# Kernel optimization log

Hardware: AMD Instinct MI355X
Metric: run time of the kernel (lower is better)

The kernel has to match this reference:

```python
import jax, jax.numpy as jnp
import numpy as np

H = 16
D_MODEL = 1024
D_K = D_MODEL // H
L = 4096


def setup_inputs() -> dict:
    key = jax.random.key(0)
    ks = jax.random.split(key, 11)
    s = 1.0 / np.sqrt(D_MODEL)
    inp = {
        "query": jax.random.normal(ks[0], (L, D_MODEL), dtype=jnp.float32),
        "key": jax.random.normal(ks[1], (L, D_MODEL), dtype=jnp.float32),
        "value": jax.random.normal(ks[2], (L, D_MODEL), dtype=jnp.float32),
        "Wq": jax.random.uniform(ks[3], (D_MODEL, D_MODEL), jnp.float32, -s, s),
        "Wk": jax.random.uniform(ks[4], (D_MODEL, D_MODEL), jnp.float32, -s, s),
        "Wv": jax.random.uniform(ks[5], (D_MODEL, D_MODEL), jnp.float32, -s, s),
        "Wo": jax.random.uniform(ks[6], (D_MODEL, D_MODEL), jnp.float32, -s, s),
        "bq": jax.random.uniform(ks[7], (D_MODEL,), jnp.float32, -s, s),
        "bk": jax.random.uniform(ks[8], (D_MODEL,), jnp.float32, -s, s),
        "bv": jax.random.uniform(ks[9], (D_MODEL,), jnp.float32, -s, s),
        "bo": jax.random.uniform(ks[10], (D_MODEL,), jnp.float32, -s, s),
    }
    return inp


def reference(query, key, value, Wq, Wk, Wv, Wo, bq, bk, bv, bo):
    # projections: torch Linear computes x @ W.T + b
    def proj(x, W, b):
        # [L, d_model] -> [h, L, d_k]
        y = x @ W.T + b
        return y.reshape(L, H, D_K).transpose(1, 0, 2)

    q = proj(query, Wq, bq)   # [h, L, d_k]
    k = proj(key, Wk, bk)
    v = proj(value, Wv, bv)

    scores = jnp.einsum("hqd,hkd->hqk", q, k) / jnp.sqrt(jnp.float32(D_K))  # [h, L, L]
    p = jax.nn.softmax(scores, axis=-1)
    x = jnp.einsum("hqk,hkd->hqd", p, v)         # [h, L, d_k]
    x = x.transpose(1, 0, 2).reshape(L, H * D_K)  # [L, d_model]
    return x @ Wo.T + bo
```

## Files before the change

kernel.cpp:

```cpp
#include <hip/hip_runtime.h>

#define L_SEQ 4096
#define DM 1024
#define NH 16
#define DK 64

typedef short s16x8 __attribute__((ext_vector_type(8)));
typedef float f32x4 __attribute__((ext_vector_type(4)));
typedef float f32x8 __attribute__((ext_vector_type(8)));
typedef float f32x16 __attribute__((ext_vector_type(16)));
typedef unsigned short u16t;
typedef unsigned int u32t;

typedef __attribute__((address_space(1))) unsigned int as1_u32;
typedef __attribute__((address_space(3))) unsigned int as3_u32;

#define GLOAD_LDS16(gsrc, ldst) \
  __builtin_amdgcn_global_load_lds((as1_u32*)(gsrc), (as3_u32*)(ldst), 16, 0, 0)

__device__ __forceinline__ u16t f2bf(float f) {
  union { float f; unsigned u; } v; v.f = f;
  unsigned u = v.u;
  u += 0x7fffu + ((u >> 16) & 1u);
  return (u16t)(u >> 16);
}

__device__ __forceinline__ float fexp2(float x) {
  float r;
  asm("v_exp_f32 %0, %1" : "=v"(r) : "v"(x));
  return r;
}

__device__ __forceinline__ float bflo(u32t u) {
  union { u32t u; float f; } v; v.u = u << 16; return v.f;
}
__device__ __forceinline__ float bfhi(u32t u) {
  union { u32t u; float f; } v; v.u = u & 0xffff0000u; return v.f;
}

struct CvtArgs { const float* s[7]; u16t* d[7]; };

__global__ __launch_bounds__(256) void cvt_all(CvtArgs a) {
  int g = blockIdx.x * 256 + threadIdx.x;
  int seg, off;
  if (g < 1572864) { seg = g >> 19;               off = g & 524287; }
  else             { int t = g - 1572864; seg = 3 + (t >> 17); off = t & 131071; }
  const float* src = a.s[seg] + (size_t)off * 8;
  u16t* dst = a.d[seg] + (size_t)off * 8;
  float4 x = *(const float4*)(src);
  float4 y = *(const float4*)(src + 4);
  uint4 o;
  o.x = (u32t)f2bf(x.x) | ((u32t)f2bf(x.y) << 16);
  o.y = (u32t)f2bf(x.z) | ((u32t)f2bf(x.w) << 16);
  o.z = (u32t)f2bf(y.x) | ((u32t)f2bf(y.y) << 16);
  o.w = (u32t)f2bf(y.z) | ((u32t)f2bf(y.w) << 16);
  *(uint4*)dst = o;
}

struct QkvArgs {
  const u16t* A[3]; const u16t* Bm[3]; const float* bias[3]; u16t* C[3];
  float scale0;
};

__global__ __launch_bounds__(256)
void gemm_qkv(QkvArgs ga) {
  __shared__ unsigned char lds[3][16384];
  const int flat = blockIdx.x;
  const int bid = (flat & 7) * 96 + (flat >> 3);
  const int z = bid >> 8;
  const int b = bid & 255;
  const int bc = (z == 2) ? (b & 31) : (b & 7);
  const int br = (z == 2) ? (b >> 5) : (b >> 3);
  const int N  = (z == 2) ? L_SEQ : DM;
  const float osc = (z == 0) ? ga.scale0 : 1.0f;
  const bool rowb = (z == 2);
  const u16t* A = ga.A[z];
  const u16t* Bm = ga.Bm[z];
  const float* bias = ga.bias[z];
  u16t* C = ga.C[z];
  const int K = DM;

  const int tid = threadIdx.x;
  const int lane = tid & 63;
  const int wv = tid >> 6;
  const int wr = wv >> 1, wc = wv & 1;
  const int l15 = lane & 15, l4 = lane >> 4;

  const int r_st = tid >> 2;
  const int c_st = (tid & 3) ^ ((r_st >> 1) & 3);
  const u16t* a0 = A + (size_t)(br * 128 + r_st) * K + c_st * 8;
  const u16t* a1 = a0 + (size_t)64 * K;
  const u16t* b0 = Bm + (size_t)(bc * 128 + r_st) * K + c_st * 8;
  const u16t* b1 = b0 + (size_t)64 * K;
  const int woff = wv * 1024;

  f32x4 acc[4][4] = {};

  auto stage = [&](int buf, int k0) {
    GLOAD_LDS16(a0 + k0, &lds[buf][woff]);
    GLOAD_LDS16(a1 + k0, &lds[buf][4096 + woff]);
    GLOAD_LDS16(b0 + k0, &lds[buf][8192 + woff]);
    GLOAD_LDS16(b1 + k0, &lds[buf][12288 + woff]);
  };

  auto compute = [&](int buf) {
    s16x8 af[4], bfr[4];
    #pragma unroll
    for (int m = 0; m < 4; ++m) {
      int r = wr * 64 + m * 16 + l15;
      int sl = l4 ^ ((r >> 1) & 3);
      af[m] = *(const s16x8*)&lds[buf][r * 64 + (sl << 4)];
    }
    #pragma unroll
    for (int n = 0; n < 4; ++n) {
      int r = wc * 64 + n * 16 + l15;
      int sl = l4 ^ ((r >> 1) & 3);
      bfr[n] = *(const s16x8*)&lds[buf][8192 + r * 64 + (sl << 4)];
    }
    #pragma unroll
    for (int m = 0; m < 4; ++m)
      #pragma unroll
      for (int n = 0; n < 4; ++n)
        acc[m][n] = __builtin_amdgcn_mfma_f32_16x16x32_bf16(af[m], bfr[n], acc[m][n], 0, 0, 0);
  };

  stage(0, 0);
  stage(1, 32);
  int t = 0;
  #pragma unroll 1
  for (int c = 0; c < 10; ++c) {
    #pragma unroll
    for (int ph = 0; ph < 3; ++ph) {
      asm volatile("s_waitcnt vmcnt(4)" ::: "memory");
      __builtin_amdgcn_s_barrier();
      __builtin_amdgcn_sched_barrier(0);
      stage((t + 2) % 3, (t + 2) * 32);
      compute(t % 3);
      ++t;
    }
  }
  asm volatile("s_waitcnt vmcnt(4)" ::: "memory");
  __builtin_amdgcn_s_barrier();
  __builtin_amdgcn_sched_barrier(0);
  compute(0);
  asm volatile("s_waitcnt vmcnt(0)" ::: "memory");
  __builtin_amdgcn_s_barrier();
  __builtin_amdgcn_sched_barrier(0);
  compute(1);

  const int l15p = rowb ? ((l15 & 3) | ((l15 & 4) << 1) | ((l15 & 8) >> 1)) : l15;

  #pragma unroll
  for (int m = 0; m < 4; ++m) {
    #pragma unroll
    for (int n = 0; n < 4; ++n) {
      #pragma unroll
      for (int i = 0; i < 4; ++i) {
        int row = br * 128 + wr * 64 + m * 16 + l4 * 4 + i;
        int col = bc * 128 + wc * 64 + n * 16 + l15p;
        float v = (acc[m][n][i] + (rowb ? bias[row] : bias[col])) * osc;
        C[(size_t)row * N + col] = f2bf(v);
      }
    }
  }
}

__global__ __launch_bounds__(256)
void gemm_out(const u16t* __restrict__ A, const u16t* __restrict__ B,
              const float* __restrict__ bias, float* __restrict__ C,
              int M, int N, int K) {
  __shared__ unsigned char lds[3][12288];
  const int tid = threadIdx.x;
  const int lane = tid & 63;
  const int wv = tid >> 6;
  const int wr = wv >> 1, wc = wv & 1;
  const int l15 = lane & 15, l4 = lane >> 4;
  const int flat = blockIdx.x + (blockIdx.y << 4);
  const int nsw = (flat & 7) * 64 + (flat >> 3);
  const int bc = nsw & 15, br = nsw >> 4;

  const int r_st = tid >> 2;
  const int c_st = (tid & 3) ^ ((r_st >> 1) & 3);
  const u16t* a0 = A + (size_t)(br * 128 + r_st) * K + c_st * 8;
  const u16t* a1 = a0 + (size_t)64 * K;
  const u16t* b0 = B + (size_t)(bc * 64 + r_st) * K + c_st * 8;
  const int woff = wv * 1024;

  f32x4 acc[4][2] = {};

  auto stage = [&](int buf, int k0) {
    GLOAD_LDS16(a0 + k0, &lds[buf][woff]);
    GLOAD_LDS16(a1 + k0, &lds[buf][4096 + woff]);
    GLOAD_LDS16(b0 + k0, &lds[buf][8192 + woff]);
  };

  auto compute = [&](int buf) {
    s16x8 af[4], bfr[2];
    #pragma unroll
    for (int m = 0; m < 4; ++m) {
      int r = wr * 64 + m * 16 + l15;
      int sl = l4 ^ ((r >> 1) & 3);
      af[m] = *(const s16x8*)&lds[buf][r * 64 + (sl << 4)];
    }
    #pragma unroll
    for (int n = 0; n < 2; ++n) {
      int r = wc * 32 + n * 16 + l15;
      int sl = l4 ^ ((r >> 1) & 3);
      bfr[n] = *(const s16x8*)&lds[buf][8192 + r * 64 + (sl << 4)];
    }
    #pragma unroll
    for (int m = 0; m < 4; ++m)
      #pragma unroll
      for (int n = 0; n < 2; ++n)
        acc[m][n] = __builtin_amdgcn_mfma_f32_16x16x32_bf16(af[m], bfr[n], acc[m][n], 0, 0, 0);
  };

  stage(0, 0);
  stage(1, 32);
  int t = 0;
  #pragma unroll 1
  for (int c = 0; c < 10; ++c) {
    #pragma unroll
    for (int ph = 0; ph < 3; ++ph) {
      asm volatile("s_waitcnt vmcnt(3)" ::: "memory");
      __builtin_amdgcn_s_barrier();
      __builtin_amdgcn_sched_barrier(0);
      stage((t + 2) % 3, (t + 2) * 32);
      compute(t % 3);
      ++t;
    }
  }
  asm volatile("s_waitcnt vmcnt(3)" ::: "memory");
  __builtin_amdgcn_s_barrier();
  __builtin_amdgcn_sched_barrier(0);
  compute(0);
  asm volatile("s_waitcnt vmcnt(0)" ::: "memory");
  __builtin_amdgcn_s_barrier();
  __builtin_amdgcn_sched_barrier(0);
  compute(1);

  #pragma unroll
  for (int m = 0; m < 4; ++m) {
    #pragma unroll
    for (int n = 0; n < 2; ++n) {
      #pragma unroll
      for (int i = 0; i < 4; ++i) {
        int row = br * 128 + wr * 64 + m * 16 + l4 * 4 + i;
        int col = bc * 64 + wc * 32 + n * 16 + l15;
        C[(size_t)row * N + col] = acc[m][n][i] + bias[col];
      }
    }
  }
}

#define PKBF(dst, a, b) \
  asm("v_cvt_pk_bf16_f32 %0, %1, %2" : "=v"(dst) : "v"(a), "v"(b))

#define MAKE_FRAG(S, B, FR) { \
    union { u32t u[4]; s16x8 v; } uu; \
    PKBF(uu.u[0], S[B + 0], S[B + 1]); \
    PKBF(uu.u[1], S[B + 2], S[B + 3]); \
    PKBF(uu.u[2], S[B + 4], S[B + 5]); \
    PKBF(uu.u[3], S[B + 6], S[B + 7]); \
    FR = uu.v; }

__global__ __launch_bounds__(512, 4)
void attn_fused(const u16t* __restrict__ Qp, const u16t* __restrict__ Kp,
                const u16t* __restrict__ VpT, u16t* __restrict__ Op,
                float* __restrict__ Ml) {
  __shared__ unsigned char sStage[3][16384];

  const int tid = threadIdx.x;
  const int lane = tid & 63;
  const int w = tid >> 6;
  const int l31 = lane & 31;
  const int hi = lane >> 5;
  const int flat = blockIdx.x;
  const int nsw = (flat & 7) * 64 + (flat >> 3);
  const int qt = nsw & 15;
  const int h = (nsw >> 4) & 15;
  const int z = nsw >> 8;
  const int kvbase = z * (L_SEQ / 2);
  const int qrow = qt * 256 + w * 32 + l31;
  u16t* Opz = Op + (size_t)z * (L_SEQ * DM);
  float* Mlz = Ml + z * (NH * L_SEQ);

  s16x8 qf[4];
  {
    const u16t* qsrc = Qp + (size_t)qrow * DM + h * DK + hi * 8;
    #pragma unroll
    for (int c = 0; c < 4; ++c) qf[c] = *(const s16x8*)(qsrc + c * 16);
  }

  f32x16 acc0 = {}, acc1 = {};
  float lrow = 0.f;

  const u16t* kptr = Kp + (size_t)(kvbase + lane) * DM + h * DK + w * 8;
  const u16t* vptr = VpT + (size_t)(h * DK + lane) * L_SEQ + kvbase + w * 8;
  const int woffK = w * 1024;

  auto stage = [&](int buf) {
    GLOAD_LDS16(kptr, &sStage[buf][woffK]);
    GLOAD_LDS16(vptr, &sStage[buf][8192 + woffK]);
    kptr += 64 * DM;
    vptr += 64;
  };

  const int rdoff = (hi << 10) + (l31 << 4);

  auto compute = [&](const unsigned char* sb) {
    f32x16 st0 = {}, st1 = {};
    __builtin_amdgcn_s_setprio(1);
    #pragma unroll
    for (int c = 0; c < 4; ++c) {
      s16x8 kf0 = *(const s16x8*)(sb + c * 2048);
      s16x8 kf1 = *(const s16x8*)(sb + c * 2048 + 512);
      st0 = __builtin_amdgcn_mfma_f32_32x32x16_bf16(kf0, qf[c], st0, 0, 0, 0);
      st1 = __builtin_amdgcn_mfma_f32_32x32x16_bf16(kf1, qf[c], st1, 0, 0, 0);
    }
    __builtin_amdgcn_s_setprio(0);

    #pragma unroll
    for (int r = 0; r < 16; ++r) {
      st0[r] = fexp2(st0[r]);
      st1[r] = fexp2(st1[r]);
    }
    f32x16 sv = st0 + st1;
    f32x8 s8v = __builtin_shufflevector(sv, sv, 0, 1, 2, 3, 4, 5, 6, 7) +
                __builtin_shufflevector(sv, sv, 8, 9, 10, 11, 12, 13, 14, 15);
    f32x4 s4v = __builtin_shufflevector(s8v, s8v, 0, 1, 2, 3) +
                __builtin_shufflevector(s8v, s8v, 4, 5, 6, 7);
    lrow += (s4v[0] + s4v[1]) + (s4v[2] + s4v[3]);

    __builtin_amdgcn_s_setprio(1);
    #pragma unroll
    for (int cc = 0; cc < 4; ++cc) {
      s16x8 pfr;
      if (cc == 0)      MAKE_FRAG(st0, 0, pfr)
      else if (cc == 1) MAKE_FRAG(st0, 8, pfr)
      else if (cc == 2) MAKE_FRAG(st1, 0, pfr)
      else              MAKE_FRAG(st1, 8, pfr)
      s16x8 vf0 = *(const s16x8*)(sb + 8192 + cc * 2048);
      s16x8 vf1 = *(const s16x8*)(sb + 8192 + cc * 2048 + 512);
      acc0 = __builtin_amdgcn_mfma_f32_32x32x16_bf16(vf0, pfr, acc0, 0, 0, 0);
      acc1 = __builtin_amdgcn_mfma_f32_32x32x16_bf16(vf1, pfr, acc1, 0, 0, 0);
    }
    __builtin_amdgcn_s_setprio(0);
  };

  auto phase = [&](int bc, int bs) {
    asm volatile("s_waitcnt vmcnt(2)" ::: "memory");
    __builtin_amdgcn_s_barrier();
    __builtin_amdgcn_sched_barrier(0);
    stage(bs);
    compute(sStage[bc] + rdoff);
  };

  stage(0);
  stage(1);
  #pragma unroll 1
  for (int c = 0; c < 10; ++c) {
    phase(0, 2);
    phase(1, 0);
    phase(2, 1);
  }
  asm volatile("s_waitcnt vmcnt(2)" ::: "memory");
  __builtin_amdgcn_s_barrier();
  __builtin_amdgcn_sched_barrier(0);
  compute(sStage[0] + rdoff);
  asm volatile("s_waitcnt vmcnt(0)" ::: "memory");
  __builtin_amdgcn_s_barrier();
  __builtin_amdgcn_sched_barrier(0);
  compute(sStage[1] + rdoff);

  lrow += __shfl_xor(lrow, 32);
  u16t* orow = Opz + (size_t)qrow * DM + h * DK;
  #pragma unroll
  for (int rq = 0; rq < 4; ++rq) {
    union { u16t h4[4]; uint2 v; } p0, p1;
    #pragma unroll
    for (int i = 0; i < 4; ++i) {
      p0.h4[i] = f2bf(acc0[4 * rq + i]);
      p1.h4[i] = f2bf(acc1[4 * rq + i]);
    }
    int d0 = 8 * rq + 4 * hi;
    *(uint2*)(orow + d0)      = p0.v;
    *(uint2*)(orow + 32 + d0) = p1.v;
  }
  if (hi == 0) Mlz[h * L_SEQ + qrow] = lrow;
}

__global__ __launch_bounds__(256)
void attn_combine(const u16t* __restrict__ Op, const float* __restrict__ Ml,
                  u16t* __restrict__ AO) {
  int g = blockIdx.x * 256 + threadIdx.x;
  int qh = g >> 2;
  int d0 = (g & 3) * 16;
  int q = qh >> 4, h = qh & 15;
  size_t off = (size_t)q * DM + h * DK + d0;
  const size_t OSTR = (size_t)L_SEQ * DM;

  int mi = h * L_SEQ + q;
  float inv = 1.0f / (Ml[mi] + Ml[NH * L_SEQ + mi]);

  uint4 a[2], b[2], o[2];
  a[0] = *(const uint4*)(Op + off);         a[1] = *(const uint4*)(Op + off + 8);
  b[0] = *(const uint4*)(Op + OSTR + off);  b[1] = *(const uint4*)(Op + OSTR + off + 8);
  #pragma unroll
  for (int k = 0; k < 2; ++k) {
    u32t* au = (u32t*)&a[k]; u32t* bu = (u32t*)&b[k]; u32t* ou = (u32t*)&o[k];
    #pragma unroll
    for (int j = 0; j < 4; ++j) {
      float lo = (bflo(au[j]) + bflo(bu[j])) * inv;
      float hf = (bfhi(au[j]) + bfhi(bu[j])) * inv;
      ou[j] = (u32t)f2bf(lo) | ((u32t)f2bf(hf) << 16);
    }
  }
  *(uint4*)(AO + off)     = o[0];
  *(uint4*)(AO + off + 8) = o[1];
}

extern "C" void kernel_launch(void* const* d_in, const int* in_sizes, int n_in,
                              void* d_out, int out_size, void* d_ws, size_t ws_size,
                              hipStream_t stream) {
  const float* query = (const float*)d_in[0];
  const float* key_  = (const float*)d_in[1];
  const float* value = (const float*)d_in[2];
  const float* Wq = (const float*)d_in[3];
  const float* Wk = (const float*)d_in[4];
  const float* Wv = (const float*)d_in[5];
  const float* Wo = (const float*)d_in[6];
  const float* bq = (const float*)d_in[7];
  const float* bk = (const float*)d_in[8];
  const float* bv = (const float*)d_in[9];
  const float* bo = (const float*)d_in[10];

  char* ws = (char*)d_ws;
  const size_t MB = 1u << 20;
  u16t* qb  = (u16t*)(ws + 0 * MB);
  u16t* kb  = (u16t*)(ws + 8 * MB);
  u16t* vb  = (u16t*)(ws + 16 * MB);
  u16t* wqb = (u16t*)(ws + 24 * MB);
  u16t* wkb = (u16t*)(ws + 26 * MB);
  u16t* wvb = (u16t*)(ws + 28 * MB);
  u16t* wob = (u16t*)(ws + 30 * MB);
  u16t* Qp  = (u16t*)(ws + 32 * MB);
  u16t* Kp  = (u16t*)(ws + 40 * MB);
  u16t* VpT = (u16t*)(ws + 48 * MB);
  u16t* AO  = (u16t*)(ws + 56 * MB);

  u16t* Op  = (u16t*)(ws + 0 * MB);
  float* Ml = (float*)(ws + 16 * MB);

  const float QSCALE = 0.125f * 1.4426950408889634f;

  CvtArgs ca;
  ca.s[0] = query; ca.s[1] = key_; ca.s[2] = value;
  ca.s[3] = Wq; ca.s[4] = Wk; ca.s[5] = Wv; ca.s[6] = Wo;
  ca.d[0] = qb; ca.d[1] = kb; ca.d[2] = vb;
  ca.d[3] = wqb; ca.d[4] = wkb; ca.d[5] = wvb; ca.d[6] = wob;
  cvt_all<<<dim3(8192), dim3(256), 0, stream>>>(ca);

  QkvArgs ga;
  ga.A[0] = qb;  ga.Bm[0] = wqb; ga.bias[0] = bq; ga.C[0] = Qp;
  ga.A[1] = kb;  ga.Bm[1] = wkb; ga.bias[1] = bk; ga.C[1] = Kp;
  ga.A[2] = wvb; ga.Bm[2] = vb;  ga.bias[2] = bv; ga.C[2] = VpT;
  ga.scale0 = QSCALE;
  gemm_qkv<<<dim3(768), dim3(256), 0, stream>>>(ga);

  attn_fused<<<dim3(512), dim3(512), 0, stream>>>(Qp, Kp, VpT, Op, Ml);

  attn_combine<<<dim3(1024), dim3(256), 0, stream>>>(Op, Ml, AO);

  gemm_out<<<dim3(DM / 64, L_SEQ / 128), dim3(256), 0, stream>>>(
      AO, wob, bo, (float*)d_out, L_SEQ, DM, DM);
}
```

Baseline: 144.8 us.

## Fuse activation fp32-to-bf16 conversion into QKV GEMM loads

The separate conversion pass over query/key/value is removed. The QKV GEMM now loads fp32 activations into registers, packs them to bf16 with v_cvt_pk_bf16_f32 and writes them to LDS, while weights still use direct global-to-LDS loads. This saves a full read and write of about 48MB of activations per call. In exchange the GEMM reads twice the activation bytes, holds more registers, and adds an LDS write plus lgkmcnt wait in every pipeline phase.

```diff
diff --git a/kernel.cpp b/kernel.cpp
--- a/kernel.cpp
+++ b/kernel.cpp
@@ -25,6 +25,12 @@
   return (u16t)(u >> 16);
 }
 
+__device__ __forceinline__ u32t pkbf(float a, float b) {
+  u32t r;
+  asm("v_cvt_pk_bf16_f32 %0, %1, %2" : "=v"(r) : "v"(a), "v"(b));
+  return r;
+}
+
 __device__ __forceinline__ float fexp2(float x) {
   float r;
   asm("v_exp_f32 %0, %1" : "=v"(r) : "v"(x));
@@ -38,13 +44,11 @@
   union { u32t u; float f; } v; v.u = u & 0xffff0000u; return v.f;
 }
 
-struct CvtArgs { const float* s[7]; u16t* d[7]; };
-
-__global__ __launch_bounds__(256) void cvt_all(CvtArgs a) {
+struct CvtWArgs { const float* s[4]; u16t* d[4]; };
+
+__global__ __launch_bounds__(256) void cvt_w(CvtWArgs a) {
   int g = blockIdx.x * 256 + threadIdx.x;
-  int seg, off;
-  if (g < 1572864) { seg = g >> 19;               off = g & 524287; }
-  else             { int t = g - 1572864; seg = 3 + (t >> 17); off = t & 131071; }
+  int seg = g >> 17, off = g & 131071;
   const float* src = a.s[seg] + (size_t)off * 8;
   u16t* dst = a.d[seg] + (size_t)off * 8;
   float4 x = *(const float4*)(src);
@@ -58,7 +62,9 @@
 }
 
 struct QkvArgs {
-  const u16t* A[3]; const u16t* Bm[3]; const float* bias[3]; u16t* C[3];
+  const float* Af[3];
+  const u16t* Wb[3];
+  const float* bias[3]; u16t* C[3];
   float scale0;
 };
 
@@ -74,8 +80,6 @@
   const int N  = (z == 2) ? L_SEQ : DM;
   const float osc = (z == 0) ? ga.scale0 : 1.0f;
   const bool rowb = (z == 2);
-  const u16t* A = ga.A[z];
-  const u16t* Bm = ga.Bm[z];
   const float* bias = ga.bias[z];
   u16t* C = ga.C[z];
   const int K = DM;
@@ -88,20 +92,22 @@
 
   const int r_st = tid >> 2;
   const int c_st = (tid & 3) ^ ((r_st >> 1) & 3);
-  const u16t* a0 = A + (size_t)(br * 128 + r_st) * K + c_st * 8;
-  const u16t* a1 = a0 + (size_t)64 * K;
-  const u16t* b0 = Bm + (size_t)(bc * 128 + r_st) * K + c_st * 8;
-  const u16t* b1 = b0 + (size_t)64 * K;
   const int woff = wv * 1024;
 
+  const float* fsrc; const u16t* gsrc;
+  int fregion, gregion;
+  if (z != 2) {
+    fsrc = ga.Af[z] + (size_t)(br * 128 + r_st) * K + c_st * 8;
+    gsrc = ga.Wb[z] + (size_t)(bc * 128 + r_st) * K + c_st * 8;
+    fregion = 0; gregion = 8192;
+  } else {
+    fsrc = ga.Af[2] + (size_t)(bc * 128 + r_st) * K + c_st * 8;
+    gsrc = ga.Wb[2] + (size_t)(br * 128 + r_st) * K + c_st * 8;
+    fregion = 8192; gregion = 0;
+  }
+
   f32x4 acc[4][4] = {};
-
-  auto stage = [&](int buf, int k0) {
-    GLOAD_LDS16(a0 + k0, &lds[buf][woff]);
-    GLOAD_LDS16(a1 + k0, &lds[buf][4096 + woff]);
-    GLOAD_LDS16(b0 + k0, &lds[buf][8192 + woff]);
-    GLOAD_LDS16(b1 + k0, &lds[buf][12288 + woff]);
-  };
+  float4 ra0[4], ra1[4];
 
   auto compute = [&](int buf) {
     s16x8 af[4], bfr[4];
@@ -124,26 +130,53 @@
         acc[m][n] = __builtin_amdgcn_mfma_f32_16x16x32_bf16(af[m], bfr[n], acc[m][n], 0, 0, 0);
   };
 
-  stage(0, 0);
-  stage(1, 32);
+#define QKV_ISSUE(S, IBUF, K0) { \
+    GLOAD_LDS16(gsrc + (K0), &lds[IBUF][gregion + woff]); \
+    GLOAD_LDS16(gsrc + (K0) + (size_t)64 * K, &lds[IBUF][gregion + 4096 + woff]); \
+    ra##S[0] = *(const float4*)(fsrc + (K0)); \
+    ra##S[1] = *(const float4*)(fsrc + (K0) + 4); \
+    ra##S[2] = *(const float4*)(fsrc + (K0) + (size_t)64 * K); \
+    ra##S[3] = *(const float4*)(fsrc + (K0) + (size_t)64 * K + 4); }
+
+#define QKV_WRITE(S, CBUF) { \
+    uint4 wA, wB; \
+    wA.x = pkbf(ra##S[0].x, ra##S[0].y); wA.y = pkbf(ra##S[0].z, ra##S[0].w); \
+    wA.z = pkbf(ra##S[1].x, ra##S[1].y); wA.w = pkbf(ra##S[1].z, ra##S[1].w); \
+    wB.x = pkbf(ra##S[2].x, ra##S[2].y); wB.y = pkbf(ra##S[2].z, ra##S[2].w); \
+    wB.z = pkbf(ra##S[3].x, ra##S[3].y); wB.w = pkbf(ra##S[3].z, ra##S[3].w); \
+    *(uint4*)(&lds[CBUF][fregion + tid * 16]) = wA; \
+    *(uint4*)(&lds[CBUF][fregion + 4096 + tid * 16]) = wB; }
+
+#define QKV_PHASE(S, CBUF, IBUF, T) { \
+    asm volatile("s_waitcnt vmcnt(6)" ::: "memory"); \
+    QKV_WRITE(S, CBUF); \
+    asm volatile("s_waitcnt lgkmcnt(0)" ::: "memory"); \
+    __builtin_amdgcn_s_barrier(); \
+    __builtin_amdgcn_sched_barrier(0); \
+    QKV_ISSUE(S, IBUF, ((T) + 2) * 32); \
+    compute(CBUF); }
+
+  QKV_ISSUE(0, 0, 0);
+  QKV_ISSUE(1, 1, 32);
   int t = 0;
   #pragma unroll 1
-  for (int c = 0; c < 10; ++c) {
-    #pragma unroll
-    for (int ph = 0; ph < 3; ++ph) {
-      asm volatile("s_waitcnt vmcnt(4)" ::: "memory");
-      __builtin_amdgcn_s_barrier();
-      __builtin_amdgcn_sched_barrier(0);
-      stage((t + 2) % 3, (t + 2) * 32);
-      compute(t % 3);
-      ++t;
-    }
-  }
-  asm volatile("s_waitcnt vmcnt(4)" ::: "memory");
+  for (int c = 0; c < 5; ++c) {
+    QKV_PHASE(0, 0, 2, t); ++t;
+    QKV_PHASE(1, 1, 0, t); ++t;
+    QKV_PHASE(0, 2, 1, t); ++t;
+    QKV_PHASE(1, 0, 2, t); ++t;
+    QKV_PHASE(0, 1, 0, t); ++t;
+    QKV_PHASE(1, 2, 1, t); ++t;
+  }
+  asm volatile("s_waitcnt vmcnt(6)" ::: "memory");
+  QKV_WRITE(0, 0);
+  asm volatile("s_waitcnt lgkmcnt(0)" ::: "memory");
   __builtin_amdgcn_s_barrier();
   __builtin_amdgcn_sched_barrier(0);
   compute(0);
   asm volatile("s_waitcnt vmcnt(0)" ::: "memory");
+  QKV_WRITE(1, 1);
+  asm volatile("s_waitcnt lgkmcnt(0)" ::: "memory");
   __builtin_amdgcn_s_barrier();
   __builtin_amdgcn_sched_barrier(0);
   compute(1);
@@ -437,9 +470,6 @@
 
   char* ws = (char*)d_ws;
   const size_t MB = 1u << 20;
-  u16t* qb  = (u16t*)(ws + 0 * MB);
-  u16t* kb  = (u16t*)(ws + 8 * MB);
-  u16t* vb  = (u16t*)(ws + 16 * MB);
   u16t* wqb = (u16t*)(ws + 24 * MB);
   u16t* wkb = (u16t*)(ws + 26 * MB);
   u16t* wvb = (u16t*)(ws + 28 * MB);
@@ -454,17 +484,16 @@
 
   const float QSCALE = 0.125f * 1.4426950408889634f;
 
-  CvtArgs ca;
-  ca.s[0] = query; ca.s[1] = key_; ca.s[2] = value;
-  ca.s[3] = Wq; ca.s[4] = Wk; ca.s[5] = Wv; ca.s[6] = Wo;
-  ca.d[0] = qb; ca.d[1] = kb; ca.d[2] = vb;
-  ca.d[3] = wqb; ca.d[4] = wkb; ca.d[5] = wvb; ca.d[6] = wob;
-  cvt_all<<<dim3(8192), dim3(256), 0, stream>>>(ca);
+  CvtWArgs cw;
+  cw.s[0] = Wq; cw.s[1] = Wk; cw.s[2] = Wv; cw.s[3] = Wo;
+  cw.d[0] = wqb; cw.d[1] = wkb; cw.d[2] = wvb; cw.d[3] = wob;
+  cvt_w<<<dim3(2048), dim3(256), 0, stream>>>(cw);
 
   QkvArgs ga;
-  ga.A[0] = qb;  ga.Bm[0] = wqb; ga.bias[0] = bq; ga.C[0] = Qp;
-  ga.A[1] = kb;  ga.Bm[1] = wkb; ga.bias[1] = bk; ga.C[1] = Kp;
-  ga.A[2] = wvb; ga.Bm[2] = vb;  ga.bias[2] = bv; ga.C[2] = VpT;
+  ga.Af[0] = query; ga.Af[1] = key_; ga.Af[2] = value;
+  ga.Wb[0] = wqb;   ga.Wb[1] = wkb;  ga.Wb[2] = wvb;
+  ga.bias[0] = bq; ga.bias[1] = bk; ga.bias[2] = bv;
+  ga.C[0] = Qp; ga.C[1] = Kp; ga.C[2] = VpT;
   ga.scale0 = QSCALE;
   gemm_qkv<<<dim3(768), dim3(256), 0, stream>>>(ga);
 
```

Result: slower. 154.2 us (+6.5%).
